# Kernel optimization log

Measured on AMD Instinct MI355X. Metric: run time of the kernel, lower is better.

The kernel has to match this reference:

```python
import jax, jax.numpy as jnp
import numpy as np

B, N, D = 8, 4096, 256
H = 8
DH = D // H          # 32 per-head dim
M = 256              # number of random features
DEPTH = 4
HID = 4 * D          # mlp hidden
EPS = 1e-6


def layernorm(x, g, b):
    mu = jnp.mean(x, axis=-1, keepdims=True)
    var = jnp.mean(jnp.square(x - mu), axis=-1, keepdims=True)
    return (x - mu) * jax.lax.rsqrt(var + EPS) * g + b


def _phi(t, proj, is_query):
    # t: (B,H,N,DH), proj: (M,DH) -> (B,H,N,M) nonnegative softmax-kernel features
    nrm = DH ** -0.25
    td = t * nrm
    u = jnp.einsum('bhnd,md->bhnm', td, proj)
    diag = 0.5 * jnp.sum(td * td, axis=-1, keepdims=True)
    if is_query:
        mx = jnp.max(u, axis=-1, keepdims=True)
    else:
        mx = jnp.max(u, axis=(-2, -1), keepdims=True)
    return (jnp.exp(u - diag - mx) + 1e-4) / jnp.sqrt(jnp.asarray(M, t.dtype))


def performer_attn(h, Wqkv, Wproj, bproj, proj):
    # h: (B,N,D)
    qkv = h @ Wqkv                                   # (B,N,3D)
    q, k, v = jnp.split(qkv, 3, axis=-1)
    to_heads = lambda t: t.reshape(B, N, H, DH).transpose(0, 2, 1, 3)
    q, k, v = to_heads(q), to_heads(k), to_heads(v)  # (B,H,N,DH)
    qp = _phi(q, proj, True)                         # (B,H,N,M)
    kp = _phi(k, proj, False)                        # (B,H,N,M)
    kv = jnp.einsum('bhnm,bhnd->bhmd', kp, v)        # (B,H,M,DH) linear-time context
    z = 1.0 / (jnp.einsum('bhnm,bhm->bhn', qp, kp.sum(axis=2)) + 1e-6)
    out = jnp.einsum('bhnm,bhmd->bhnd', qp, kv) * z[..., None]
    out = out.transpose(0, 2, 1, 3).reshape(B, N, D)
    return out @ Wproj + bproj


def mlp(h, W1, b1, W2, b2):
    return jax.nn.gelu(h @ W1 + b1, approximate=False) @ W2 + b2


def setup_inputs() -> dict:
    key = jax.random.key(0)
    ks = jax.random.split(key, 10)
    inp = {
        'x': jax.random.normal(ks[0], (B, N, D), jnp.float32),
        'pos_emb': 0.02 * jax.random.normal(ks[1], (N, D), jnp.float32),
        'g1n': jnp.ones((D,), jnp.float32),
        'b1n': jnp.zeros((D,), jnp.float32),
        'g2n': jnp.ones((D,), jnp.float32),
        'b2n': jnp.zeros((D,), jnp.float32),
        'Wqkv': 0.02 * jax.random.normal(ks[2], (DEPTH, D, 3 * D), jnp.float32),
        'Wproj': 0.02 * jax.random.normal(ks[3], (DEPTH, D, D), jnp.float32),
        'bproj': jnp.zeros((DEPTH, D), jnp.float32),
        'W1': 0.02 * jax.random.normal(ks[4], (DEPTH, D, HID), jnp.float32),
        'b1m': jnp.zeros((DEPTH, HID), jnp.float32),
        'W2': 0.02 * jax.random.normal(ks[5], (DEPTH, HID, D), jnp.float32),
        'b2m': jnp.zeros((DEPTH, D), jnp.float32),
        'proj_mat': jax.random.normal(ks[6], (DEPTH, M, DH), jnp.float32),
    }
    return inp


def reference(x, pos_emb, g1n, b1n, g2n, b2n, Wqkv, Wproj, bproj, W1, b1m, W2, b2m, proj_mat):
    h = x + pos_emb[None]
    for l in range(DEPTH):  # small fixed depth
        h = h + performer_attn(layernorm(h, g1n, b1n), Wqkv[l], Wproj[l], bproj[l], proj_mat[l])
        h = h + mlp(layernorm(h, g2n, b2n), W1[l], b1m[l], W2[l], b2m[l])
    return h
```

## Files before the change

kernel.cpp:

```cpp
#include <hip/hip_runtime.h>
#include <hip/hip_bf16.h>
#include <math.h>

#define B 8
#define N 4096
#define D 256
#define H 8
#define DH 32
#define M 256
#define DEPTH 4
#define HID 1024
#define NRM 0.4204482076268573f

typedef __attribute__((ext_vector_type(8))) short short8;
typedef __attribute__((ext_vector_type(4))) float f32x4;

static __device__ __forceinline__ unsigned short f2bf(float f) {
    __hip_bfloat16 h = __float2bfloat16(f);
    return __builtin_bit_cast(unsigned short, h);
}
static __device__ __forceinline__ float bfu2f(unsigned short u) {
    unsigned int x = ((unsigned int)u) << 16;
    return __builtin_bit_cast(float, x);
}
static __device__ __forceinline__ float gelu_fast(float x) {
    float z = 0.7978845608028654f * (x + 0.044715f * x * x * x);
    float e = __expf(2.0f * z);
    float th = 1.0f - 2.0f / (e + 1.0f);
    return 0.5f * x * (1.0f + th);
}

__global__ void add_pos_kernel(const float* __restrict__ x, const float* __restrict__ pos,
                               float* __restrict__ h) {
    int i = blockIdx.x * 256 + threadIdx.x;
    int nd = i % (N * D);
    h[i] = x[i] + pos[nd];
}

__global__ void projbf_kernel(const float* __restrict__ in, unsigned short* __restrict__ out) {
    int i = blockIdx.x * 256 + threadIdx.x;
    out[i] = f2bf(in[i]);
}

__global__ __launch_bounds__(256) void wtrans_kernel(const float* __restrict__ in,
                                                     unsigned short* __restrict__ out,
                                                     int Kd, int Nd, int slim) {
    __shared__ float tl[32][33];
    int n0 = blockIdx.x * 32, k0 = blockIdx.y * 32;
    int t = threadIdx.x;
    int kk = t >> 3, c4 = (t & 7) * 4;
    float4 v = *reinterpret_cast<const float4*>(&in[(size_t)(k0 + kk) * Nd + n0 + c4]);
    tl[kk][c4 + 0] = v.x; tl[kk][c4 + 1] = v.y; tl[kk][c4 + 2] = v.z; tl[kk][c4 + 3] = v.w;
    __syncthreads();
    int nn = t >> 3, k4 = (t & 7) * 4;
    float sc = (n0 + nn < slim) ? NRM : 1.0f;
    ushort4 o;
    o.x = f2bf(tl[k4 + 0][nn] * sc); o.y = f2bf(tl[k4 + 1][nn] * sc);
    o.z = f2bf(tl[k4 + 2][nn] * sc); o.w = f2bf(tl[k4 + 3][nn] * sc);
    *reinterpret_cast<ushort4*>(&out[(size_t)(n0 + nn) * Kd + k0 + k4]) = o;
}

__global__ __launch_bounds__(256) void ln_kernel(const float* __restrict__ in,
                                                 const float* __restrict__ g,
                                                 const float* __restrict__ bb,
                                                 unsigned short* __restrict__ out) {
    int wave = threadIdx.x >> 6, lane = threadIdx.x & 63;
    long row = (long)blockIdx.x * 4 + wave;
    float4 v = reinterpret_cast<const float4*>(in + row * D)[lane];
    float s = v.x + v.y + v.z + v.w;
#pragma unroll
    for (int o = 32; o >= 1; o >>= 1) s += __shfl_xor(s, o);
    float mu = s * (1.0f / D);
    float d0 = v.x - mu, d1 = v.y - mu, d2 = v.z - mu, d3 = v.w - mu;
    float ss = d0 * d0 + d1 * d1 + d2 * d2 + d3 * d3;
#pragma unroll
    for (int o = 32; o >= 1; o >>= 1) ss += __shfl_xor(ss, o);
    float inv = rsqrtf(ss * (1.0f / D) + 1e-6f);
    float4 gv = reinterpret_cast<const float4*>(g)[lane];
    float4 bv = reinterpret_cast<const float4*>(bb)[lane];
    ushort4 o4;
    o4.x = f2bf(d0 * inv * gv.x + bv.x);
    o4.y = f2bf(d1 * inv * gv.y + bv.y);
    o4.z = f2bf(d2 * inv * gv.z + bv.z);
    o4.w = f2bf(d3 * inv * gv.w + bv.w);
    *reinterpret_cast<ushort4*>(&out[row * D + lane * 4]) = o4;
}

template <int NK, bool BIAS, bool GELU_ACT, bool RESID, bool OUT16>
__global__ __launch_bounds__(256) void mgemm_kernel(const unsigned short* __restrict__ A,
                                                    const unsigned short* __restrict__ Bt,
                                                    const float* __restrict__ bias,
                                                    float* __restrict__ C,
                                                    unsigned short* __restrict__ O16,
                                                    int Nc) {
    const int K = NK * 64;
    __shared__ __align__(16) short Als[2][128][64];
    __shared__ __align__(16) short Bls[2][128][64];
    int t = threadIdx.x;
    int l = t & 63, w = t >> 6;
    int wr = w >> 1, wc = w & 1;
    int nwg = gridDim.x * gridDim.y;
    int bid = blockIdx.y * gridDim.x + blockIdx.x;
    int lgid = (bid & 7) * (nwg >> 3) + (bid >> 3);
    int bx = lgid % gridDim.x;
    int by = lgid / gridDim.x;
    long m0 = (long)by * 128;
    int n0 = bx * 128;
    int lr = l & 15;
    int lg = l >> 4;
    int srow = t >> 1, half = t & 1;

    const unsigned short* Ap = &A[(size_t)(m0 + srow) * K + half * 32];
    const unsigned short* Bp = &Bt[(size_t)(n0 + srow) * K + half * 32];

    short* awp[4];
    short* bwp[4];
    short* awp1[4];
    short* bwp1[4];
#pragma unroll
    for (int i = 0; i < 4; i++) {
        int cw = ((half * 4 + i) ^ (srow & 7)) * 8;
        awp[i] = &Als[0][srow][cw];
        bwp[i] = &Bls[0][srow][cw];
        awp1[i] = &Als[1][srow][cw];
        bwp1[i] = &Bls[1][srow][cw];
    }

    short8 ra[4], rb[4];
#pragma unroll
    for (int i = 0; i < 4; i++) {
        ra[i] = *reinterpret_cast<const short8*>(Ap + i * 8);
        rb[i] = *reinterpret_cast<const short8*>(Bp + i * 8);
    }
#pragma unroll
    for (int i = 0; i < 4; i++) {
        *reinterpret_cast<short8*>(awp[i]) = ra[i];
        *reinterpret_cast<short8*>(bwp[i]) = rb[i];
    }
    if (NK > 1) {
#pragma unroll
        for (int i = 0; i < 4; i++) {
            ra[i] = *reinterpret_cast<const short8*>(Ap + 64 + i * 8);
            rb[i] = *reinterpret_cast<const short8*>(Bp + 64 + i * 8);
        }
    }
    __syncthreads();

    f32x4 acc[4][4];
#pragma unroll
    for (int i = 0; i < 4; i++)
#pragma unroll
        for (int j = 0; j < 4; j++) acc[i][j] = (f32x4){0.f, 0.f, 0.f, 0.f};

#pragma unroll
    for (int it = 0; it < NK; it++) {
        int buf = it & 1;
        short8 a[4][2], b[4][2];
#pragma unroll
        for (int i = 0; i < 4; i++) {
            int row = wr * 64 + i * 16 + lr;
#pragma unroll
            for (int ks = 0; ks < 2; ks++) {
                int cr = ((ks * 4 + lg) ^ (lr & 7)) * 8;
                a[i][ks] = *reinterpret_cast<const short8*>(&Als[buf][row][cr]);
            }
        }
#pragma unroll
        for (int j = 0; j < 4; j++) {
            int row = wc * 64 + j * 16 + lr;
#pragma unroll
            for (int ks = 0; ks < 2; ks++) {
                int cr = ((ks * 4 + lg) ^ (lr & 7)) * 8;
                b[j][ks] = *reinterpret_cast<const short8*>(&Bls[buf][row][cr]);
            }
        }
        if (it + 1 < NK) {
#pragma unroll
            for (int i = 0; i < 4; i++) {
                if (buf == 0) {
                    *reinterpret_cast<short8*>(awp1[i]) = ra[i];
                    *reinterpret_cast<short8*>(bwp1[i]) = rb[i];
                } else {
                    *reinterpret_cast<short8*>(awp[i]) = ra[i];
                    *reinterpret_cast<short8*>(bwp[i]) = rb[i];
                }
            }
            if (it + 2 < NK) {
                int ko = (it + 2) * 64;
#pragma unroll
                for (int i = 0; i < 4; i++) {
                    ra[i] = *reinterpret_cast<const short8*>(Ap + ko + i * 8);
                    rb[i] = *reinterpret_cast<const short8*>(Bp + ko + i * 8);
                }
            }
        }
#pragma unroll
        for (int ks = 0; ks < 2; ks++)
#pragma unroll
            for (int i = 0; i < 4; i++)
#pragma unroll
                for (int j = 0; j < 4; j++)
                    acc[i][j] = __builtin_amdgcn_mfma_f32_16x16x32_bf16(b[j][ks], a[i][ks],
                                                                       acc[i][j], 0, 0, 0);
        __syncthreads();
    }

    float4 bias4[4];
    if (BIAS) {
#pragma unroll
        for (int j = 0; j < 4; j++)
            bias4[j] = *reinterpret_cast<const float4*>(&bias[n0 + wc * 64 + j * 16 + lg * 4]);
    }
#pragma unroll
    for (int i = 0; i < 4; i++) {
        long grow = m0 + wr * 64 + i * 16 + lr;
#pragma unroll
        for (int j = 0; j < 4; j++) {
            int gcol = n0 + wc * 64 + j * 16 + lg * 4;
            f32x4 v = acc[i][j];
            if (BIAS) {
                v[0] += bias4[j].x; v[1] += bias4[j].y; v[2] += bias4[j].z; v[3] += bias4[j].w;
            }
            if (GELU_ACT) {
#pragma unroll
                for (int r = 0; r < 4; r++) v[r] = gelu_fast(v[r]);
            }
            if (OUT16) {
                short4 o;
                o.x = (short)f2bf(v[0]); o.y = (short)f2bf(v[1]);
                o.z = (short)f2bf(v[2]); o.w = (short)f2bf(v[3]);
                *reinterpret_cast<short4*>(&O16[grow * Nc + gcol]) = o;
            } else if (RESID) {
                float4 c0 = *reinterpret_cast<const float4*>(&C[grow * Nc + gcol]);
                c0.x += v[0]; c0.y += v[1]; c0.z += v[2]; c0.w += v[3];
                *reinterpret_cast<float4*>(&C[grow * Nc + gcol]) = c0;
            } else {
                float4 c0 = {v[0], v[1], v[2], v[3]};
                *reinterpret_cast<float4*>(&C[grow * Nc + gcol]) = c0;
            }
        }
    }
}

#define KV_P 16
#define KV_ROWS (N / KV_P)
#define PSZ 8484
__global__ __launch_bounds__(256) void kv_kernel(const unsigned short* __restrict__ qkv16,
                                                 const unsigned short* __restrict__ projbf,
                                                 float* __restrict__ kvp) {
    __shared__ __align__(16) unsigned short kp_s[256][64];
    __shared__ __align__(16) unsigned short vT_s[32][66];
    __shared__ float red[4];
    __shared__ float asumred[4][256];
    __shared__ float vred[256][4];
    int t = threadIdx.x;
    int l = t & 63, w = t >> 6;
    int lr = l & 15, lg = l >> 4;
    int bh = blockIdx.x, b = bh >> 3, h = bh & 7;
    int n0 = blockIdx.y * KV_ROWS;
    int rsw = (lr & 7) << 3;

    f32x4 kvacc[4][2];
#pragma unroll
    for (int mf = 0; mf < 4; mf++)
#pragma unroll
        for (int dd = 0; dd < 2; dd++) kvacc[mf][dd] = (f32x4){0.f, 0.f, 0.f, 0.f};
    float asum_p[16];
#pragma unroll
    for (int f = 0; f < 16; f++) asum_p[f] = 0.f;
    float4 vs4 = {0.f, 0.f, 0.f, 0.f};
    float cmax = -1e30f;

    for (int c = 0; c < KV_ROWS / 64; c++) {
        __syncthreads();
        size_t kbase = ((size_t)(b * N) + n0 + c * 64 + w * 16 + lr) * 768 + 256 + h * 32 + lg * 8;
        short8 aq = *reinterpret_cast<const short8*>(qkv16 + kbase);
        float sq = 0.f;
#pragma unroll
        for (int e = 0; e < 8; e++) {
            float xx = bfu2f((unsigned short)aq[e]);
            sq += xx * xx;
        }
        sq += __shfl_xor(sq, 16);
        sq += __shfl_xor(sq, 32);
        float dgr[4];
#pragma unroll
        for (int r = 0; r < 4; r++) dgr[r] = 0.5f * __shfl(sq, lg * 4 + r);
        int cbase = (w * 16 + lg * 4) ^ rsw;
#pragma unroll
        for (int f = 0; f < 16; f++) {
            short8 bq = *reinterpret_cast<const short8*>(projbf + (f * 16 + lr) * 32 + lg * 8);
            f32x4 u = __builtin_amdgcn_mfma_f32_16x16x32_bf16(aq, bq, (f32x4){0.f, 0.f, 0.f, 0.f}, 0, 0, 0);
            cmax = fmaxf(cmax, fmaxf(fmaxf(u[0], u[1]), fmaxf(u[2], u[3])));
            float p0 = __expf(u[0] - dgr[0]);
            float p1 = __expf(u[1] - dgr[1]);
            float p2 = __expf(u[2] - dgr[2]);
            float p3 = __expf(u[3] - dgr[3]);
            asum_p[f] += p0 + p1 + p2 + p3;
            short4 o;
            o.x = (short)f2bf(p0); o.y = (short)f2bf(p1);
            o.z = (short)f2bf(p2); o.w = (short)f2bf(p3);
            *reinterpret_cast<short4*>(&kp_s[f * 16 + lr][cbase]) = o;
        }
#pragma unroll
        for (int ii = 0; ii < 2; ii++) {
            int idx = t + ii * 256;
            int nn = idx >> 3, dz = (idx & 7) * 4;
            const unsigned short* vp =
                qkv16 + ((size_t)(b * N) + n0 + c * 64 + nn) * 768 + 512 + h * 32 + dz;
            short4 vv = *reinterpret_cast<const short4*>(vp);
            float v0 = bfu2f((unsigned short)vv.x), v1 = bfu2f((unsigned short)vv.y);
            float v2 = bfu2f((unsigned short)vv.z), v3 = bfu2f((unsigned short)vv.w);
            vs4.x += v0; vs4.y += v1; vs4.z += v2; vs4.w += v3;
            vT_s[dz + 0][nn] = (unsigned short)vv.x; vT_s[dz + 1][nn] = (unsigned short)vv.y;
            vT_s[dz + 2][nn] = (unsigned short)vv.z; vT_s[dz + 3][nn] = (unsigned short)vv.w;
        }
        __syncthreads();
#pragma unroll
        for (int ks = 0; ks < 2; ks++) {
            short8 bv0 = *reinterpret_cast<const short8*>(&vT_s[lr][ks * 32 + lg * 8]);
            short8 bv1 = *reinterpret_cast<const short8*>(&vT_s[16 + lr][ks * 32 + lg * 8]);
#pragma unroll
            for (int mf = 0; mf < 4; mf++) {
                short8 am = *reinterpret_cast<const short8*>(
                    &kp_s[w * 64 + mf * 16 + lr][(ks * 32 + lg * 8) ^ rsw]);
                kvacc[mf][0] = __builtin_amdgcn_mfma_f32_16x16x32_bf16(am, bv0, kvacc[mf][0], 0, 0, 0);
                kvacc[mf][1] = __builtin_amdgcn_mfma_f32_16x16x32_bf16(am, bv1, kvacc[mf][1], 0, 0, 0);
            }
        }
    }
#pragma unroll
    for (int f = 0; f < 16; f++) {
        asum_p[f] += __shfl_xor(asum_p[f], 16);
        asum_p[f] += __shfl_xor(asum_p[f], 32);
    }
    if (l < 16) {
#pragma unroll
        for (int f = 0; f < 16; f++) asumred[w][f * 16 + l] = asum_p[f];
    }
    vred[t][0] = vs4.x; vred[t][1] = vs4.y; vred[t][2] = vs4.z; vred[t][3] = vs4.w;
#pragma unroll
    for (int o = 1; o < 64; o <<= 1) cmax = fmaxf(cmax, __shfl_xor(cmax, o));
    if (l == 0) red[w] = cmax;
    __syncthreads();
    size_t base = ((size_t)bh * KV_P + blockIdx.y) * PSZ;
#pragma unroll
    for (int mf = 0; mf < 4; mf++)
#pragma unroll
        for (int dd = 0; dd < 2; dd++) {
            int m = w * 64 + mf * 16 + lg * 4;
            int d = dd * 16 + lr;
            float4 o;
            o.x = kvacc[mf][dd][0]; o.y = kvacc[mf][dd][1];
            o.z = kvacc[mf][dd][2]; o.w = kvacc[mf][dd][3];
            *reinterpret_cast<float4*>(&kvp[base + (size_t)d * 256 + m]) = o;
        }
    {
        float s = asumred[0][t] + asumred[1][t] + asumred[2][t] + asumred[3][t];
        kvp[base + 8192 + t] = s;
    }
    if (t < 32) {
        int f4g = t >> 2, cc = t & 3;
        float s = 0.f;
#pragma unroll
        for (int g = 0; g < 32; g++) s += vred[g * 8 + f4g][cc];
        kvp[base + 8448 + t] = s;
    }
    if (t == 0) kvp[base + 8480] = fmaxf(fmaxf(red[0], red[1]), fmaxf(red[2], red[3]));
}

__global__ __launch_bounds__(256) void kv_combine_kernel(const float* __restrict__ kvp,
                                                         unsigned short* __restrict__ kvTb,
                                                         float* __restrict__ ksumf) {
    __shared__ float vst[32];
    int t = threadIdx.x;
    int bh = blockIdx.x >> 2, dq = blockIdx.x & 3;
    size_t base0 = (size_t)bh * KV_P * PSZ;
    float gm = -1e30f;
#pragma unroll
    for (int p = 0; p < KV_P; p++) gm = fmaxf(gm, kvp[base0 + p * PSZ + 8480]);
    if (t < 32) {
        float s = 0.f;
#pragma unroll
        for (int p = 0; p < KV_P; p++) s += kvp[base0 + p * PSZ + 8448 + t];
        vst[t] = s;
    }
    __syncthreads();
    float es = __expf(-gm);
    int d = dq * 8 + (t >> 5);
    int m0 = (t & 31) * 8;
    float4 a0 = {0.f, 0.f, 0.f, 0.f}, a1 = {0.f, 0.f, 0.f, 0.f};
#pragma unroll
    for (int p = 0; p < KV_P; p++) {
        const float* src = &kvp[base0 + p * PSZ + (size_t)d * 256 + m0];
        float4 x0 = *reinterpret_cast<const float4*>(src);
        float4 x1 = *reinterpret_cast<const float4*>(src + 4);
        a0.x += x0.x; a0.y += x0.y; a0.z += x0.z; a0.w += x0.w;
        a1.x += x1.x; a1.y += x1.y; a1.z += x1.z; a1.w += x1.w;
    }
    float vadd = 1e-4f * vst[d];
    ushort4 o0, o1;
    o0.x = f2bf((a0.x * es + vadd) * 0.0625f); o0.y = f2bf((a0.y * es + vadd) * 0.0625f);
    o0.z = f2bf((a0.z * es + vadd) * 0.0625f); o0.w = f2bf((a0.w * es + vadd) * 0.0625f);
    o1.x = f2bf((a1.x * es + vadd) * 0.0625f); o1.y = f2bf((a1.y * es + vadd) * 0.0625f);
    o1.z = f2bf((a1.z * es + vadd) * 0.0625f); o1.w = f2bf((a1.w * es + vadd) * 0.0625f);
    *reinterpret_cast<ushort4*>(&kvTb[((size_t)bh * 32 + d) * 256 + m0]) = o0;
    *reinterpret_cast<ushort4*>(&kvTb[((size_t)bh * 32 + d) * 256 + m0 + 4]) = o1;
    if (dq == 0) {
        float S = 0.f;
#pragma unroll
        for (int p = 0; p < KV_P; p++) S += kvp[base0 + p * PSZ + 8192 + t];
        ksumf[bh * 256 + t] = (S * es + 1e-4f * (float)N) * 0.0625f;
    }
}

#define ATT_TILES 8
__global__ __launch_bounds__(256) void attn_kernel(const unsigned short* __restrict__ qkv16,
                                                   const unsigned short* __restrict__ projbf,
                                                   const unsigned short* __restrict__ kvTb,
                                                   const float* __restrict__ ksumf,
                                                   unsigned short* __restrict__ attn16) {
    __shared__ __align__(16) unsigned short qp_s[64 * 256];
    int t = threadIdx.x;
    int l = t & 63, w = t >> 6;
    int lr = l & 15, lg = l >> 4;
    int bh = blockIdx.x, b = bh >> 3, h = bh & 7;
    int swz = (lr & 7) << 3;
    int row = w * 16 + lr;

    const unsigned short* kvb = kvTb + (size_t)bh * 32 * 256;
    short8 kva0[8], kva1[8];
#pragma unroll
    for (int k0 = 0; k0 < 8; k0++) {
        kva0[k0] = *reinterpret_cast<const short8*>(kvb + (size_t)lr * 256 + k0 * 32 + lg * 8);
        kva1[k0] = *reinterpret_cast<const short8*>(kvb + (size_t)(16 + lr) * 256 + k0 * 32 + lg * 8);
    }

    int tile0 = blockIdx.y * ATT_TILES;
    size_t qstep = (size_t)64 * 768;
    size_t qbase = ((size_t)(b * N) + tile0 * 64 + w * 16 + lr) * 768 + h * 32 + lg * 8;
    short8 qf = *reinterpret_cast<const short8*>(qkv16 + qbase);

    for (int tl = 0; tl < ATT_TILES; tl++) {
        short8 qfn = qf;
        if (tl < ATT_TILES - 1)
            qfn = *reinterpret_cast<const short8*>(qkv16 + qbase + (size_t)(tl + 1) * qstep);

        float sq = 0.f;
#pragma unroll
        for (int e = 0; e < 8; e++) {
            float xx = bfu2f((unsigned short)qf[e]);
            sq += xx * xx;
        }
        sq += __shfl_xor(sq, 16);
        sq += __shfl_xor(sq, 32);
        float dg = 0.5f * sq;

        f32x4 ua[16];
#pragma unroll
        for (int f = 0; f < 16; f++) {
            short8 bq = *reinterpret_cast<const short8*>(projbf + (f * 16 + lr) * 32 + lg * 8);
            ua[f] = __builtin_amdgcn_mfma_f32_16x16x32_bf16(bq, qf, (f32x4){0.f, 0.f, 0.f, 0.f}, 0, 0, 0);
        }

        float mx = -1e30f;
#pragma unroll
        for (int f = 0; f < 16; f++)
#pragma unroll
            for (int r = 0; r < 4; r++) mx = fmaxf(mx, ua[f][r]);
        mx = fmaxf(mx, __shfl_xor(mx, 16));
        mx = fmaxf(mx, __shfl_xor(mx, 32));

        float zs = 0.f;
#pragma unroll
        for (int f = 0; f < 16; f++) {
            float4 ks4 = *reinterpret_cast<const float4*>(&ksumf[bh * 256 + f * 16 + lg * 4]);
            float p0 = (__expf(ua[f][0] - dg - mx) + 1e-4f) * 0.0625f;
            float p1 = (__expf(ua[f][1] - dg - mx) + 1e-4f) * 0.0625f;
            float p2 = (__expf(ua[f][2] - dg - mx) + 1e-4f) * 0.0625f;
            float p3 = (__expf(ua[f][3] - dg - mx) + 1e-4f) * 0.0625f;
            zs += p0 * ks4.x + p1 * ks4.y + p2 * ks4.z + p3 * ks4.w;
            short4 o;
            o.x = (short)f2bf(p0); o.y = (short)f2bf(p1);
            o.z = (short)f2bf(p2); o.w = (short)f2bf(p3);
            *reinterpret_cast<short4*>(&qp_s[row * 256 + ((f * 16 + lg * 4) ^ swz)]) = o;
        }
        zs += __shfl_xor(zs, 16);
        zs += __shfl_xor(zs, 32);
        float zf = 1.0f / (zs + 1e-6f);

        f32x4 oacc[2];
        oacc[0] = (f32x4){0.f, 0.f, 0.f, 0.f};
        oacc[1] = (f32x4){0.f, 0.f, 0.f, 0.f};
#pragma unroll
        for (int k0 = 0; k0 < 8; k0++) {
            short8 qpf = *reinterpret_cast<const short8*>(
                &qp_s[row * 256 + ((k0 * 32 + lg * 8) ^ swz)]);
            oacc[0] = __builtin_amdgcn_mfma_f32_16x16x32_bf16(kva0[k0], qpf, oacc[0], 0, 0, 0);
            oacc[1] = __builtin_amdgcn_mfma_f32_16x16x32_bf16(kva1[k0], qpf, oacc[1], 0, 0, 0);
        }
        size_t orow = ((size_t)(b * N) + (tile0 + tl) * 64 + w * 16 + lr) * 256 + h * 32;
#pragma unroll
        for (int dd = 0; dd < 2; dd++) {
            short4 o;
            o.x = (short)f2bf(oacc[dd][0] * zf);
            o.y = (short)f2bf(oacc[dd][1] * zf);
            o.z = (short)f2bf(oacc[dd][2] * zf);
            o.w = (short)f2bf(oacc[dd][3] * zf);
            *reinterpret_cast<short4*>(&attn16[orow + dd * 16 + lg * 4]) = o;
        }
        qf = qfn;
    }
}

extern "C" void kernel_launch(void* const* d_in, const int* in_sizes, int n_in,
                              void* d_out, int out_size, void* d_ws, size_t ws_size,
                              hipStream_t stream) {
    const float* x = (const float*)d_in[0];
    const float* pos = (const float*)d_in[1];
    const float* g1 = (const float*)d_in[2];
    const float* b1 = (const float*)d_in[3];
    const float* g2 = (const float*)d_in[4];
    const float* b2 = (const float*)d_in[5];
    const float* Wqkv = (const float*)d_in[6];
    const float* Wproj = (const float*)d_in[7];
    const float* bproj = (const float*)d_in[8];
    const float* W1 = (const float*)d_in[9];
    const float* b1m = (const float*)d_in[10];
    const float* W2 = (const float*)d_in[11];
    const float* b2m = (const float*)d_in[12];
    const float* projm = (const float*)d_in[13];

    float* h = (float*)d_out;
    char* p = (char*)d_ws;
    auto alloc = [&](size_t bytes) { char* r = p; p += (bytes + 255) & ~(size_t)255; return r; };
    unsigned short* wbf    = (unsigned short*)alloc((size_t)DEPTH * 786432 * 2);
    unsigned short* projb  = (unsigned short*)alloc((size_t)DEPTH * M * DH * 2);
    unsigned short* ln16   = (unsigned short*)alloc((size_t)B * N * D * 2);
    unsigned short* qkv16  = (unsigned short*)alloc((size_t)B * N * HID * 2);
    unsigned short* hid16  = qkv16;
    unsigned short* attn16 = (unsigned short*)alloc((size_t)B * N * D * 2);
    float* kvp             = (float*)alloc((size_t)64 * KV_P * PSZ * 4);
    unsigned short* kvTb   = (unsigned short*)alloc((size_t)64 * 32 * 256 * 2);
    float* ksumf           = (float*)alloc((size_t)64 * 256 * 4);

    for (int l = 0; l < DEPTH; l++) {
        size_t lb = (size_t)l * 786432;
        wtrans_kernel<<<dim3(768 / 32, 256 / 32), 256, 0, stream>>>(
            Wqkv + (size_t)l * D * 3 * D, wbf + lb + 0, 256, 768, 512);
        wtrans_kernel<<<dim3(256 / 32, 256 / 32), 256, 0, stream>>>(
            Wproj + (size_t)l * D * D, wbf + lb + 196608, 256, 256, 0);
        wtrans_kernel<<<dim3(1024 / 32, 256 / 32), 256, 0, stream>>>(
            W1 + (size_t)l * D * HID, wbf + lb + 262144, 256, 1024, 0);
        wtrans_kernel<<<dim3(256 / 32, 1024 / 32), 256, 0, stream>>>(
            W2 + (size_t)l * HID * D, wbf + lb + 524288, 1024, 256, 0);
    }
    projbf_kernel<<<DEPTH * M * DH / 256, 256, 0, stream>>>(projm, projb);

    add_pos_kernel<<<B * N * D / 256, 256, 0, stream>>>(x, pos, h);

    for (int l = 0; l < DEPTH; l++) {
        size_t lb = (size_t)l * 786432;
        const unsigned short* wqT = wbf + lb + 0;
        const unsigned short* wpT = wbf + lb + 196608;
        const unsigned short* w1T = wbf + lb + 262144;
        const unsigned short* w2T = wbf + lb + 524288;
        const float* bp = bproj + (size_t)l * D;
        const float* b1l = b1m + (size_t)l * HID;
        const float* b2l = b2m + (size_t)l * D;
        const unsigned short* prb = projb + (size_t)l * M * DH;

        ln_kernel<<<B * N / 4, 256, 0, stream>>>(h, g1, b1, ln16);
        mgemm_kernel<4, false, false, false, true><<<dim3(768 / 128, B * N / 128), 256, 0, stream>>>(
            ln16, wqT, nullptr, nullptr, qkv16, 768);
        kv_kernel<<<dim3(B * H, KV_P), 256, 0, stream>>>(qkv16, prb, kvp);
        kv_combine_kernel<<<B * H * 4, 256, 0, stream>>>(kvp, kvTb, ksumf);
        attn_kernel<<<dim3(B * H, (N / 64) / ATT_TILES), 256, 0, stream>>>(
            qkv16, prb, kvTb, ksumf, attn16);
        mgemm_kernel<4, true, false, true, false><<<dim3(256 / 128, B * N / 128), 256, 0, stream>>>(
            attn16, wpT, bp, h, nullptr, 256);
        ln_kernel<<<B * N / 4, 256, 0, stream>>>(h, g2, b2, ln16);
        mgemm_kernel<4, true, true, false, true><<<dim3(1024 / 128, B * N / 128), 256, 0, stream>>>(
            ln16, w1T, b1l, nullptr, hid16, 1024);
        mgemm_kernel<16, true, false, true, false><<<dim3(256 / 128, B * N / 128), 256, 0, stream>>>(
            hid16, w2T, b2l, h, nullptr, 256);
    }
}
```

Measured before the change: 904.1 us.

## Fuse MLP up-projection, GELU and down-projection into one kernel

Replaces the two MLP GEMM launches with a single kernel that, for each 64-row tile, computes 128-column chunks of the hidden activation, applies bias and GELU, stages the result in shared memory, and immediately accumulates the down-projection into registers before adding into the residual. This avoids writing and re-reading the bf16 hidden tensor in global memory. In exchange, weights are read straight from global memory without shared-memory tiling, each block streams the full W1 and W2, and there are only 512 blocks with heavy register use, which may limit occupancy and weight reuse.

```diff
diff --git a/kernel.cpp b/kernel.cpp
--- a/kernel.cpp
+++ b/kernel.cpp
@@ -242,6 +242,114 @@
     }
 }
 
+__global__ __launch_bounds__(256) void mlp_fused_kernel(const unsigned short* __restrict__ ln16,
+                                                        const unsigned short* __restrict__ w1T,
+                                                        const unsigned short* __restrict__ w2T,
+                                                        const float* __restrict__ b1,
+                                                        const float* __restrict__ b2,
+                                                        float* __restrict__ hres) {
+    __shared__ __align__(16) unsigned short A_s[64][256];
+    __shared__ __align__(16) unsigned short t1_s[2][64][128];
+    int t = threadIdx.x;
+    int l = t & 63, w = t >> 6;
+    int lr = l & 15, lg = l >> 4;
+    int r7 = lr & 7;
+    long m0 = (long)blockIdx.x * 64;
+
+    {
+        int row = t >> 2, q = t & 3, rs = row & 7;
+        const unsigned short* src = ln16 + (size_t)(m0 + row) * 256 + q * 64;
+#pragma unroll
+        for (int i = 0; i < 8; i++) {
+            short8 v = *reinterpret_cast<const short8*>(src + i * 8);
+            *reinterpret_cast<short8*>(&A_s[row][((q * 8 + i) ^ rs) * 8]) = v;
+        }
+    }
+    __syncthreads();
+
+    f32x4 oacc[4][4];
+#pragma unroll
+    for (int i = 0; i < 4; i++)
+#pragma unroll
+        for (int j = 0; j < 4; j++) oacc[i][j] = (f32x4){0.f, 0.f, 0.f, 0.f};
+
+    for (int c = 0; c < HID / 128; c++) {
+        int cb = c & 1;
+        f32x4 acc1[4][2];
+#pragma unroll
+        for (int mf = 0; mf < 4; mf++)
+#pragma unroll
+            for (int nh = 0; nh < 2; nh++) acc1[mf][nh] = (f32x4){0.f, 0.f, 0.f, 0.f};
+#pragma unroll
+        for (int ks = 0; ks < 8; ks++) {
+            short8 af[4];
+#pragma unroll
+            for (int mf = 0; mf < 4; mf++)
+                af[mf] = *reinterpret_cast<const short8*>(
+                    &A_s[mf * 16 + lr][(((ks * 4 + lg) ^ r7)) * 8]);
+#pragma unroll
+            for (int nh = 0; nh < 2; nh++) {
+                short8 wf = *reinterpret_cast<const short8*>(
+                    &w1T[(size_t)(c * 128 + w * 32 + nh * 16 + lr) * 256 + ks * 32 + lg * 8]);
+#pragma unroll
+                for (int mf = 0; mf < 4; mf++)
+                    acc1[mf][nh] = __builtin_amdgcn_mfma_f32_16x16x32_bf16(wf, af[mf],
+                                                                          acc1[mf][nh], 0, 0, 0);
+            }
+        }
+#pragma unroll
+        for (int nh = 0; nh < 2; nh++) {
+            float4 b1v = *reinterpret_cast<const float4*>(&b1[c * 128 + w * 32 + nh * 16 + lg * 4]);
+#pragma unroll
+            for (int mf = 0; mf < 4; mf++) {
+                f32x4 v = acc1[mf][nh];
+                v[0] = gelu_fast(v[0] + b1v.x);
+                v[1] = gelu_fast(v[1] + b1v.y);
+                v[2] = gelu_fast(v[2] + b1v.z);
+                v[3] = gelu_fast(v[3] + b1v.w);
+                short4 o;
+                o.x = (short)f2bf(v[0]); o.y = (short)f2bf(v[1]);
+                o.z = (short)f2bf(v[2]); o.w = (short)f2bf(v[3]);
+                int col = (w * 32 + nh * 16 + lg * 4) ^ (r7 * 8);
+                *reinterpret_cast<short4*>(&t1_s[cb][mf * 16 + lr][col]) = o;
+            }
+        }
+        __syncthreads();
+#pragma unroll
+        for (int ks = 0; ks < 4; ks++) {
+            short8 tf[4];
+#pragma unroll
+            for (int mf = 0; mf < 4; mf++)
+                tf[mf] = *reinterpret_cast<const short8*>(
+                    &t1_s[cb][mf * 16 + lr][(ks * 32 + lg * 8) ^ (r7 * 8)]);
+#pragma unroll
+            for (int nf = 0; nf < 4; nf++) {
+                short8 wf = *reinterpret_cast<const short8*>(
+                    &w2T[(size_t)(w * 64 + nf * 16 + lr) * 1024 + c * 128 + ks * 32 + lg * 8]);
+#pragma unroll
+                for (int mf = 0; mf < 4; mf++)
+                    oacc[mf][nf] = __builtin_amdgcn_mfma_f32_16x16x32_bf16(wf, tf[mf],
+                                                                          oacc[mf][nf], 0, 0, 0);
+            }
+        }
+    }
+
+#pragma unroll
+    for (int nf = 0; nf < 4; nf++) {
+        float4 b2v = *reinterpret_cast<const float4*>(&b2[w * 64 + nf * 16 + lg * 4]);
+#pragma unroll
+        for (int mf = 0; mf < 4; mf++) {
+            float* hp = &hres[(size_t)(m0 + mf * 16 + lr) * 256 + w * 64 + nf * 16 + lg * 4];
+            float4 c0 = *reinterpret_cast<const float4*>(hp);
+            c0.x += oacc[mf][nf][0] + b2v.x;
+            c0.y += oacc[mf][nf][1] + b2v.y;
+            c0.z += oacc[mf][nf][2] + b2v.z;
+            c0.w += oacc[mf][nf][3] + b2v.w;
+            *reinterpret_cast<float4*>(hp) = c0;
+        }
+    }
+}
+
 #define KV_P 16
 #define KV_ROWS (N / KV_P)
 #define PSZ 8484
@@ -538,7 +646,6 @@
     unsigned short* projb  = (unsigned short*)alloc((size_t)DEPTH * M * DH * 2);
     unsigned short* ln16   = (unsigned short*)alloc((size_t)B * N * D * 2);
     unsigned short* qkv16  = (unsigned short*)alloc((size_t)B * N * HID * 2);
-    unsigned short* hid16  = qkv16;
     unsigned short* attn16 = (unsigned short*)alloc((size_t)B * N * D * 2);
     float* kvp             = (float*)alloc((size_t)64 * KV_P * PSZ * 4);
     unsigned short* kvTb   = (unsigned short*)alloc((size_t)64 * 32 * 256 * 2);
@@ -580,9 +687,6 @@
         mgemm_kernel<4, true, false, true, false><<<dim3(256 / 128, B * N / 128), 256, 0, stream>>>(
             attn16, wpT, bp, h, nullptr, 256);
         ln_kernel<<<B * N / 4, 256, 0, stream>>>(h, g2, b2, ln16);
-        mgemm_kernel<4, true, true, false, true><<<dim3(1024 / 128, B * N / 128), 256, 0, stream>>>(
-            ln16, w1T, b1l, nullptr, hid16, 1024);
-        mgemm_kernel<16, true, false, true, false><<<dim3(256 / 128, B * N / 128), 256, 0, stream>>>(
-            hid16, w2T, b2l, h, nullptr, 256);
-    }
-}
+        mlp_fused_kernel<<<B * N / 64, 256, 0, stream>>>(ln16, w1T, w2T, b1l, b2l, h);
+    }
+}
```

Result: slower. 1.008 ms (+11.5%).
